# Kernel tuning notes

Measured on AMD Instinct MI355X. Metric: run time of the kernel, lower is better.

The kernel has to match this reference:

```python
import jax, jax.numpy as jnp
import numpy as np
import math

H = 4
D_MODEL = 512
OUT_DIM = D_MODEL // 2  # 256 (concat=True path)
D_K = OUT_DIM // H      # 64
N = 4096


def setup_inputs() -> dict:
    key0 = jax.random.key(0)
    ks = jax.random.split(key0, 12)
    s = 1.0 / math.sqrt(D_MODEL)
    inp = {
        "query": jax.random.normal(ks[0], (N, D_MODEL), dtype=jnp.float32),
        "key": jax.random.normal(ks[1], (N, D_MODEL), dtype=jnp.float32),
        "mask": jax.random.randint(ks[2], (N, N), 0, 2, dtype=jnp.int32),
        # 4 linears (q, k, q_v, k_v), each d_model -> out_dim
        "Wq": jax.random.normal(ks[3], (OUT_DIM, D_MODEL), dtype=jnp.float32) * s,
        "bq": jax.random.normal(ks[4], (OUT_DIM,), dtype=jnp.float32) * s,
        "Wk": jax.random.normal(ks[5], (OUT_DIM, D_MODEL), dtype=jnp.float32) * s,
        "bk": jax.random.normal(ks[6], (OUT_DIM,), dtype=jnp.float32) * s,
        "Wqv": jax.random.normal(ks[7], (OUT_DIM, D_MODEL), dtype=jnp.float32) * s,
        "bqv": jax.random.normal(ks[8], (OUT_DIM,), dtype=jnp.float32) * s,
        "Wkv": jax.random.normal(ks[9], (OUT_DIM, D_MODEL), dtype=jnp.float32) * s,
        "bkv": jax.random.normal(ks[10], (OUT_DIM,), dtype=jnp.float32) * s,
    }
    return inp


def _heads(x, W, b):
    # [N, d_model] @ W^T + b -> [N, out_dim] -> [h, N, d_k]
    y = x @ W.T + b
    return y.reshape(-1, H, D_K).transpose(1, 0, 2)


def reference(query, key, mask, Wq, bq, Wk, bk, Wqv, bqv, Wkv, bkv):
    q = _heads(query, Wq, bq)    # [h, Nq, d_k]
    k = _heads(key, Wk, bk)      # [h, Nk, d_k]
    qv = _heads(query, Wqv, bqv)  # [h, Nq, d_k]
    kv = _heads(key, Wkv, bkv)    # [h, Nk, d_k]

    scores = jnp.einsum("hqd,hkd->hqk", q, k) / math.sqrt(D_K)  # [h, Nq, Nk]
    scores = jnp.where(mask[None] == 0, jnp.float32(-1e9), scores)
    p = jax.nn.softmax(scores, axis=-1)  # attention weights per head

    # x1 = ELU(p @ k_v), x2 = ELU(p^T @ q_v); concat over heads.
    x1 = jax.nn.elu(jnp.einsum("hqk,hkd->hqd", p, kv))  # [h, Nq, d_k]
    x2 = jax.nn.elu(jnp.einsum("hqk,hqd->hkd", p, qv))  # [h, Nk, d_k]
    x1 = x1.transpose(1, 0, 2).reshape(-1, H * D_K)  # [Nq, out_dim]
    x2 = x2.transpose(1, 0, 2).reshape(-1, H * D_K)  # [Nk, out_dim]
    # Dropout omitted (inference / deterministic reference).
    return x1, x2, p
```

## Files before the change

kernel.cpp:

```cpp
#include <hip/hip_runtime.h>
#include <hip/hip_bf16.h>

#define NN 4096
#define DMODEL 512
#define ODIM 256
#define NHEAD 4
#define DKH 64
#define NKW 64

typedef __attribute__((ext_vector_type(8))) short short8;
typedef __attribute__((ext_vector_type(4))) short short4v;
typedef __attribute__((ext_vector_type(8))) __bf16 bf16x8;
typedef __attribute__((ext_vector_type(4))) float f32x4;

__device__ __forceinline__ short f2bf(float f) {
    unsigned u = __builtin_bit_cast(unsigned, f);
    u += 0x7fffu + ((u >> 16) & 1u);
    return (short)(u >> 16);
}
__device__ __forceinline__ float bf2f(short s) {
    unsigned u = ((unsigned)(unsigned short)s) << 16;
    return __builtin_bit_cast(float, u);
}
__device__ __forceinline__ f32x4 mfma16(short8 a, short8 b, f32x4 c) {
    return __builtin_amdgcn_mfma_f32_16x16x32_bf16(
        __builtin_bit_cast(bf16x8, a), __builtin_bit_cast(bf16x8, b), c, 0, 0, 0);
}

__global__ __launch_bounds__(256) void pack_mask_k(const int* __restrict__ mask,
                                                   unsigned long long* __restrict__ bits) {
    int tid = blockIdx.x * 256 + threadIdx.x;
    int wid = tid >> 6;
    int lane = tid & 63;
    int v = __builtin_nontemporal_load(mask + (size_t)wid * 64 + lane);
    unsigned long long b = __ballot(v != 0);
    if (lane == 0) bits[wid] = b;
}

__global__ __launch_bounds__(256) void proj_k(
    const float* __restrict__ Xq, const float* __restrict__ Xk,
    const float* __restrict__ Wq, const float* __restrict__ bq,
    const float* __restrict__ Wk, const float* __restrict__ bk,
    const float* __restrict__ Wqv, const float* __restrict__ bqv,
    const float* __restrict__ Wkv, const float* __restrict__ bkv,
    short* __restrict__ qh, short* __restrict__ kh,
    short* __restrict__ qvT, short* __restrict__ kvT) {
    int z = blockIdx.z;
    const float *X, *W, *B;
    short* out;
    int tr;
    float postscale = 1.f;
    switch (z) {
        case 0: X = Xq; W = Wq;  B = bq;  out = qh;  tr = 0; postscale = 0.125f; break;
        case 1: X = Xk; W = Wk;  B = bk;  out = kh;  tr = 0; break;
        case 2: X = Xq; W = Wqv; B = bqv; out = qvT; tr = 1; break;
        default: X = Xk; W = Wkv; B = bkv; out = kvT; tr = 1; break;
    }
    int lane = threadIdx.x & 63, w = threadIdx.x >> 6;
    int lr = lane & 15, lg = lane >> 4;
    int m0 = blockIdx.x * 64 + (w >> 1) * 32;
    int n0 = blockIdx.y * 64 + (w & 1) * 32;

    f32x4 acc[2][2] = {};
    for (int kk = 0; kk < DMODEL; kk += 32) {
        short8 a[2], b[2];
#pragma unroll
        for (int i = 0; i < 2; i++) {
            const float* pa = X + (size_t)(m0 + i * 16 + lr) * DMODEL + kk + lg * 8;
            const float* pb = W + (size_t)(n0 + i * 16 + lr) * DMODEL + kk + lg * 8;
            float4 a0 = *(const float4*)pa;
            float4 a1 = *(const float4*)(pa + 4);
            float4 b0 = *(const float4*)pb;
            float4 b1 = *(const float4*)(pb + 4);
            a[i][0] = f2bf(a0.x); a[i][1] = f2bf(a0.y); a[i][2] = f2bf(a0.z); a[i][3] = f2bf(a0.w);
            a[i][4] = f2bf(a1.x); a[i][5] = f2bf(a1.y); a[i][6] = f2bf(a1.z); a[i][7] = f2bf(a1.w);
            b[i][0] = f2bf(b0.x); b[i][1] = f2bf(b0.y); b[i][2] = f2bf(b0.z); b[i][3] = f2bf(b0.w);
            b[i][4] = f2bf(b1.x); b[i][5] = f2bf(b1.y); b[i][6] = f2bf(b1.z); b[i][7] = f2bf(b1.w);
        }
#pragma unroll
        for (int i = 0; i < 2; i++)
#pragma unroll
            for (int j = 0; j < 2; j++) acc[i][j] = mfma16(a[i], b[j], acc[i][j]);
    }
#pragma unroll
    for (int i = 0; i < 2; i++)
#pragma unroll
        for (int j = 0; j < 2; j++) {
            int col = n0 + j * 16 + lr;
            float bv = B[col];
            int hh = col >> 6, dk = col & 63;
#pragma unroll
            for (int r = 0; r < 4; r++) {
                int row = m0 + i * 16 + lg * 4 + r;
                short s = f2bf((acc[i][j][r] + bv) * postscale);
                if (!tr) out[((size_t)hh * NN + row) * DKH + dk] = s;
                else     out[((size_t)hh * DKH + dk) * NN + row] = s;
            }
        }
}

__global__ __launch_bounds__(512) void attn_fused_k(
    const short* __restrict__ qh, const short* __restrict__ kh, const short* __restrict__ kvT,
    const unsigned long long* __restrict__ bits,
    short* __restrict__ pbuf, float* __restrict__ linv_ws,
    float* __restrict__ x1_out, float* __restrict__ p_out) {
    int h = blockIdx.y;
    int strip = blockIdx.x;
    int tid = threadIdx.x, lane = tid & 63, w = tid >> 6;
    int lr = lane & 15, lg = lane >> 4;
    int q0 = strip * 16;

    __shared__ float smemf[4608];
    short (*plds)[16][72] = (short (*)[16][72])smemf;
    float (*xbuf)[64][17] = (float (*)[64][17])smemf;
    __shared__ float sl[8][16];
    __shared__ float linv_s[16];

    const short* khh = kh + (size_t)h * NN * DKH;
    const unsigned long long* brow = bits + (size_t)(q0 + lr) * NKW;
    short* ptile0 = pbuf + (((size_t)(h * 256 + strip) * 64) << 10);

    short8 bq[2];
#pragma unroll
    for (int kk = 0; kk < 2; kk++)
        bq[kk] = *(const short8*)(qh + ((size_t)h * NN + q0 + lr) * DKH + kk * 32 + lg * 8);

    float lrun = 0.f;
    f32x4 acc1[4] = {};
    for (int t = 0; t < 8; t++) {
        int kt = w * 8 + t;
        f32x4 s[4] = {};
#pragma unroll
        for (int fj = 0; fj < 4; fj++)
#pragma unroll
            for (int kk = 0; kk < 2; kk++) {
                short8 a = *(const short8*)(khh + (size_t)(kt * 64 + fj * 16 + lr) * DKH + kk * 32 + lg * 8);
                s[fj] = mfma16(a, bq[kk], s[fj]);
            }
        unsigned long long mw = brow[kt] >> (lg * 4);
#pragma unroll
        for (int fj = 0; fj < 4; fj++) {
            short4v pb4;
#pragma unroll
            for (int r = 0; r < 4; r++) {
                bool keep = (mw >> (fj * 16 + r)) & 1ull;
                float e = __expf(keep ? s[fj][r] : -100.f);
                lrun += e;
                pb4[r] = f2bf(e);
            }
            *(short4v*)&plds[w][lr][fj * 16 + lg * 4] = pb4;
        }
#pragma unroll
        for (int kk = 0; kk < 2; kk++) {
            short8 a1 = *(const short8*)&plds[w][lr][kk * 32 + lg * 8];
#pragma unroll
            for (int fd = 0; fd < 4; fd++) {
                short8 bv = *(const short8*)(kvT + ((size_t)h * DKH + fd * 16 + lr) * NN + kt * 64 + kk * 32 + lg * 8);
                acc1[fd] = mfma16(a1, bv, acc1[fd]);
            }
        }
        {
            short8 v0, v1;
#pragma unroll
            for (int j = 0; j < 8; j++) v0[j] = plds[w][j][lane];
#pragma unroll
            for (int j = 0; j < 8; j++) v1[j] = plds[w][8 + j][lane];
            short* ptile = ptile0 + ((size_t)kt << 10) + lane * 16;
            *(short8*)(ptile) = v0;
            *(short8*)(ptile + 8) = v1;
        }
    }
    lrun += __shfl_xor(lrun, 16);
    lrun += __shfl_xor(lrun, 32);
    if (lg == 0) sl[w][lr] = lrun;
    __syncthreads();
    float l = 0.f;
#pragma unroll
    for (int w2 = 0; w2 < 8; w2++) l += sl[w2][lr];
    float linv = l > 0.f ? 1.f / l : 0.f;
    if (w == 0 && lg == 0) {
        linv_s[lr] = linv;
        linv_ws[(size_t)h * NN + q0 + lr] = linv;
    }
    __syncthreads();

    asm volatile("s_waitcnt vmcnt(0)" ::: "memory");
    float linvv[16];
#pragma unroll
    for (int j = 0; j < 16; j++) linvv[j] = linv_s[j];
    const short* tl0 = ptile0 + ((size_t)(w * 8) << 10) + lane * 16;
    short8 pv0 = *(const short8*)(tl0);
    short8 pv1 = *(const short8*)(tl0 + 8);
    for (int t = 0; t < 8; t++) {
        int kt = w * 8 + t;
        short8 n0 = pv0, n1 = pv1;
        if (t < 7) {
            const short* tn = ptile0 + ((size_t)(kt + 1) << 10) + lane * 16;
            n0 = *(const short8*)(tn);
            n1 = *(const short8*)(tn + 8);
        }
        float* pd = p_out + ((size_t)h * NN + q0) * NN + kt * 64 + lane;
#pragma unroll
        for (int j = 0; j < 8; j++) pd[(size_t)j * NN] = bf2f(pv0[j]) * linvv[j];
#pragma unroll
        for (int j = 0; j < 8; j++) pd[(size_t)(8 + j) * NN] = bf2f(pv1[j]) * linvv[8 + j];
        pv0 = n0; pv1 = n1;
    }

    __syncthreads();
    if (w >= 4) {
#pragma unroll
        for (int fd = 0; fd < 4; fd++)
#pragma unroll
            for (int r = 0; r < 4; r++) xbuf[w - 4][lane][fd * 4 + r] = acc1[fd][r];
    }
    __syncthreads();
    if (w < 4) {
#pragma unroll
        for (int fd = 0; fd < 4; fd++)
#pragma unroll
            for (int r = 0; r < 4; r++) acc1[fd][r] += xbuf[w][lane][fd * 4 + r];
    }
    __syncthreads();
    if (w >= 1 && w < 4) {
#pragma unroll
        for (int fd = 0; fd < 4; fd++)
#pragma unroll
            for (int r = 0; r < 4; r++) xbuf[w - 1][lane][fd * 4 + r] = acc1[fd][r];
    }
    __syncthreads();
    if (w == 0) {
#pragma unroll
        for (int fd = 0; fd < 4; fd++)
#pragma unroll
            for (int r = 0; r < 4; r++) {
                float v = acc1[fd][r] + xbuf[0][lane][fd * 4 + r] + xbuf[1][lane][fd * 4 + r] +
                          xbuf[2][lane][fd * 4 + r];
                v *= linv_s[lg * 4 + r];
                v = v > 0.f ? v : (__expf(v) - 1.f);
                x1_out[(size_t)(q0 + lg * 4 + r) * ODIM + h * DKH + fd * 16 + lr] = v;
            }
    }
}

__global__ __launch_bounds__(256) void scale_qv_k(const short* __restrict__ qvT,
                                                  const float* __restrict__ linv,
                                                  short* __restrict__ qvS) {
    int idx = blockIdx.x * 256 + threadIdx.x;
    int q8 = idx & 511;
    int dh = idx >> 9;
    int h = dh >> 6;
    short8 v = *(const short8*)(qvT + (size_t)dh * NN + q8 * 8);
    const float* lp = linv + (size_t)h * NN + q8 * 8;
    float4 l0 = *(const float4*)lp;
    float4 l1 = *(const float4*)(lp + 4);
    short8 o;
    o[0] = f2bf(bf2f(v[0]) * l0.x); o[1] = f2bf(bf2f(v[1]) * l0.y);
    o[2] = f2bf(bf2f(v[2]) * l0.z); o[3] = f2bf(bf2f(v[3]) * l0.w);
    o[4] = f2bf(bf2f(v[4]) * l1.x); o[5] = f2bf(bf2f(v[5]) * l1.y);
    o[6] = f2bf(bf2f(v[6]) * l1.z); o[7] = f2bf(bf2f(v[7]) * l1.w);
    *(short8*)(qvS + (size_t)dh * NN + q8 * 8) = o;
}

__global__ __launch_bounds__(512) void px2b_k(
    const short* __restrict__ pbuf, const short* __restrict__ qvS,
    float* __restrict__ x2part) {
    int kt = blockIdx.x, h = blockIdx.y, z = blockIdx.z;
    int tid = threadIdx.x, lane = tid & 63, w = tid >> 6;
    int fj = w & 3, sh = w >> 2;
    int lr = lane & 15, lg = lane >> 4;

    __shared__ float red[4][64][17];

    const short* qvh = qvS + (size_t)h * DKH * NN;
    f32x4 acc[4] = {};
    int qbase = z * 1024 + sh * 512;

    int qq0 = qbase;
    int strip0 = (qq0 >> 4) + (lg >> 1);
    short8 afc = *(const short8*)(pbuf + (((size_t)(h * 256 + strip0) * 64 + kt) << 10) +
                                  (fj * 16 + lr) * 16 + (lg & 1) * 8);
    short8 bvc0 = *(const short8*)(qvh + (size_t)(0 * 16 + lr) * NN + qq0 + lg * 8);
    short8 bvc1 = *(const short8*)(qvh + (size_t)(1 * 16 + lr) * NN + qq0 + lg * 8);
    short8 bvc2 = *(const short8*)(qvh + (size_t)(2 * 16 + lr) * NN + qq0 + lg * 8);
    short8 bvc3 = *(const short8*)(qvh + (size_t)(3 * 16 + lr) * NN + qq0 + lg * 8);

    for (int it = 0; it < 16; it++) {
        short8 afn = afc, bvn0 = bvc0, bvn1 = bvc1, bvn2 = bvc2, bvn3 = bvc3;
        if (it < 15) {
            int qq = qbase + (it + 1) * 32;
            int strip = (qq >> 4) + (lg >> 1);
            afn = *(const short8*)(pbuf + (((size_t)(h * 256 + strip) * 64 + kt) << 10) +
                                   (fj * 16 + lr) * 16 + (lg & 1) * 8);
            bvn0 = *(const short8*)(qvh + (size_t)(0 * 16 + lr) * NN + qq + lg * 8);
            bvn1 = *(const short8*)(qvh + (size_t)(1 * 16 + lr) * NN + qq + lg * 8);
            bvn2 = *(const short8*)(qvh + (size_t)(2 * 16 + lr) * NN + qq + lg * 8);
            bvn3 = *(const short8*)(qvh + (size_t)(3 * 16 + lr) * NN + qq + lg * 8);
        }
        acc[0] = mfma16(afc, bvc0, acc[0]);
        acc[1] = mfma16(afc, bvc1, acc[1]);
        acc[2] = mfma16(afc, bvc2, acc[2]);
        acc[3] = mfma16(afc, bvc3, acc[3]);
        afc = afn; bvc0 = bvn0; bvc1 = bvn1; bvc2 = bvn2; bvc3 = bvn3;
    }
    if (sh == 1) {
#pragma unroll
        for (int fd = 0; fd < 4; fd++)
#pragma unroll
            for (int r = 0; r < 4; r++) red[fj][lane][fd * 4 + r] = acc[fd][r];
    }
    __syncthreads();
    if (sh == 0) {
        float* xp = x2part + (size_t)z * NN * ODIM;
#pragma unroll
        for (int fd = 0; fd < 4; fd++)
#pragma unroll
            for (int r = 0; r < 4; r++) {
                float v = acc[fd][r] + red[fj][lane][fd * 4 + r];
                xp[(size_t)(kt * 64 + fj * 16 + lg * 4 + r) * ODIM + h * DKH + fd * 16 + lr] = v;
            }
    }
}

__global__ __launch_bounds__(256) void combine_x2_k(const float* __restrict__ x2part,
                                                    float* __restrict__ x2_out) {
    int idx = blockIdx.x * 256 + threadIdx.x;
    size_t i = (size_t)idx * 4;
    const size_t stride = (size_t)NN * ODIM;
    float4 a = *(const float4*)(x2part + i);
    float4 b = *(const float4*)(x2part + stride + i);
    float4 c = *(const float4*)(x2part + 2 * stride + i);
    float4 d = *(const float4*)(x2part + 3 * stride + i);
    float4 o;
    o.x = a.x + b.x + c.x + d.x;
    o.y = a.y + b.y + c.y + d.y;
    o.z = a.z + b.z + c.z + d.z;
    o.w = a.w + b.w + c.w + d.w;
    o.x = o.x > 0.f ? o.x : (__expf(o.x) - 1.f);
    o.y = o.y > 0.f ? o.y : (__expf(o.y) - 1.f);
    o.z = o.z > 0.f ? o.z : (__expf(o.z) - 1.f);
    o.w = o.w > 0.f ? o.w : (__expf(o.w) - 1.f);
    *(float4*)(x2_out + i) = o;
}

__global__ __launch_bounds__(512) void attn_fb_k(
    const short* __restrict__ qh, const short* __restrict__ kh, const short* __restrict__ kvT,
    const unsigned long long* __restrict__ bits,
    float* __restrict__ x1_out, float* __restrict__ p_out) {
    int h = blockIdx.y;
    int tid = threadIdx.x, lane = tid & 63, w = tid >> 6;
    int lr = lane & 15, lg = lane >> 4;
    int q0 = blockIdx.x * 16;

    __shared__ float smemf[4608];
    short (*plds)[16][72] = (short (*)[16][72])smemf;
    float (*xbuf)[64][17] = (float (*)[64][17])smemf;
    __shared__ float sl[8][16];

    const short* khh = kh + (size_t)h * NN * DKH;
    const unsigned long long* brow = bits + (size_t)(q0 + lr) * NKW;

    short8 bq[2];
#pragma unroll
    for (int kk = 0; kk < 2; kk++)
        bq[kk] = *(const short8*)(qh + ((size_t)h * NN + q0 + lr) * DKH + kk * 32 + lg * 8);

    float lrun = 0.f;
    for (int t = 0; t < 8; t++) {
        int kt = w * 8 + t;
        f32x4 s[4] = {};
#pragma unroll
        for (int fj = 0; fj < 4; fj++)
#pragma unroll
            for (int kk = 0; kk < 2; kk++) {
                short8 a = *(const short8*)(khh + (size_t)(kt * 64 + fj * 16 + lr) * DKH + kk * 32 + lg * 8);
                s[fj] = mfma16(a, bq[kk], s[fj]);
            }
        unsigned long long mw = brow[kt] >> (lg * 4);
#pragma unroll
        for (int fj = 0; fj < 4; fj++)
#pragma unroll
            for (int r = 0; r < 4; r++) {
                bool keep = (mw >> (fj * 16 + r)) & 1ull;
                lrun += __expf(keep ? s[fj][r] : -100.f);
            }
    }
    lrun += __shfl_xor(lrun, 16);
    lrun += __shfl_xor(lrun, 32);
    if (lg == 0) sl[w][lr] = lrun;
    __syncthreads();
    float l = 0.f;
#pragma unroll
    for (int w2 = 0; w2 < 8; w2++) l += sl[w2][lr];
    float linv = l > 0.f ? 1.f / l : 0.f;

    f32x4 acc1[4] = {};
    float* prow = p_out + ((size_t)h * NN + q0 + lr) * NN;
    for (int t = 0; t < 8; t++) {
        int kt = w * 8 + t;
        f32x4 s[4] = {};
#pragma unroll
        for (int fj = 0; fj < 4; fj++)
#pragma unroll
            for (int kk = 0; kk < 2; kk++) {
                short8 a = *(const short8*)(khh + (size_t)(kt * 64 + fj * 16 + lr) * DKH + kk * 32 + lg * 8);
                s[fj] = mfma16(a, bq[kk], s[fj]);
            }
        unsigned long long mw = brow[kt] >> (lg * 4);
#pragma unroll
        for (int fj = 0; fj < 4; fj++) {
            float4 pv;
            short4v pb;
#pragma unroll
            for (int r = 0; r < 4; r++) {
                bool keep = (mw >> (fj * 16 + r)) & 1ull;
                float p = __expf(keep ? s[fj][r] : -100.f) * linv;
                (&pv.x)[r] = p;
                pb[r] = f2bf(p);
            }
            *(float4*)(prow + kt * 64 + fj * 16 + lg * 4) = pv;
            *(short4v*)&plds[w][lr][fj * 16 + lg * 4] = pb;
        }
#pragma unroll
        for (int kk = 0; kk < 2; kk++) {
            short8 a1 = *(const short8*)&plds[w][lr][kk * 32 + lg * 8];
#pragma unroll
            for (int fd = 0; fd < 4; fd++) {
                short8 bv = *(const short8*)(kvT + ((size_t)h * DKH + fd * 16 + lr) * NN + kt * 64 + kk * 32 + lg * 8);
                acc1[fd] = mfma16(a1, bv, acc1[fd]);
            }
        }
    }
    __syncthreads();
    if (w >= 4) {
#pragma unroll
        for (int fd = 0; fd < 4; fd++)
#pragma unroll
            for (int r = 0; r < 4; r++) xbuf[w - 4][lane][fd * 4 + r] = acc1[fd][r];
    }
    __syncthreads();
    if (w < 4) {
#pragma unroll
        for (int fd = 0; fd < 4; fd++)
#pragma unroll
            for (int r = 0; r < 4; r++) acc1[fd][r] += xbuf[w][lane][fd * 4 + r];
    }
    __syncthreads();
    if (w >= 1 && w < 4) {
#pragma unroll
        for (int fd = 0; fd < 4; fd++)
#pragma unroll
            for (int r = 0; r < 4; r++) xbuf[w - 1][lane][fd * 4 + r] = acc1[fd][r];
    }
    __syncthreads();
    if (w == 0) {
#pragma unroll
        for (int fd = 0; fd < 4; fd++)
#pragma unroll
            for (int r = 0; r < 4; r++) {
                float v = acc1[fd][r] + xbuf[0][lane][fd * 4 + r] + xbuf[1][lane][fd * 4 + r] +
                          xbuf[2][lane][fd * 4 + r];
                v = v > 0.f ? v : (__expf(v) - 1.f);
                x1_out[(size_t)(q0 + lg * 4 + r) * ODIM + h * DKH + fd * 16 + lr] = v;
            }
    }
}

__global__ __launch_bounds__(512) void px2_fb_k(
    const float* __restrict__ p, const short* __restrict__ qvT,
    float* __restrict__ x2_out) {
    int h = blockIdx.y;
    int k0 = blockIdx.x * 32;
    int tid = threadIdx.x, lane = tid & 63, w = tid >> 6;
    int lr = lane & 15, lg = lane >> 4;

    __shared__ float red[4][64][33];

    f32x4 acc[2][4] = {};
    const float* pbase = p + (size_t)h * NN * NN;
    const short* qvh = qvT + (size_t)h * DKH * NN;

    for (int it = 0; it < 16; it++) {
        int qq = w * 512 + it * 32;
        short8 aP[2];
#pragma unroll
        for (int fj = 0; fj < 2; fj++) {
            const float* pp = pbase + (size_t)(qq + lg * 8) * NN + k0 + fj * 16 + lr;
            short8 av;
#pragma unroll
            for (int j = 0; j < 8; j++) av[j] = f2bf(pp[j * NN]);
            aP[fj] = av;
        }
#pragma unroll
        for (int fd = 0; fd < 4; fd++) {
            short8 bv = *(const short8*)(qvh + (size_t)(fd * 16 + lr) * NN + qq + lg * 8);
#pragma unroll
            for (int fj = 0; fj < 2; fj++) acc[fj][fd] = mfma16(aP[fj], bv, acc[fj][fd]);
        }
    }
    if (w >= 4) {
#pragma unroll
        for (int fj = 0; fj < 2; fj++)
#pragma unroll
            for (int fd = 0; fd < 4; fd++)
#pragma unroll
                for (int r = 0; r < 4; r++)
                    red[w - 4][lane][fj * 16 + fd * 4 + r] = acc[fj][fd][r];
    }
    __syncthreads();
    if (w < 4) {
#pragma unroll
        for (int fj = 0; fj < 2; fj++)
#pragma unroll
            for (int fd = 0; fd < 4; fd++)
#pragma unroll
                for (int r = 0; r < 4; r++)
                    acc[fj][fd][r] += red[w][lane][fj * 16 + fd * 4 + r];
    }
    __syncthreads();
    if (w >= 1 && w < 4) {
#pragma unroll
        for (int fj = 0; fj < 2; fj++)
#pragma unroll
            for (int fd = 0; fd < 4; fd++)
#pragma unroll
                for (int r = 0; r < 4; r++)
                    red[w - 1][lane][fj * 16 + fd * 4 + r] = acc[fj][fd][r];
    }
    __syncthreads();
    if (w == 0) {
#pragma unroll
        for (int fj = 0; fj < 2; fj++)
#pragma unroll
            for (int fd = 0; fd < 4; fd++)
#pragma unroll
                for (int r = 0; r < 4; r++) {
                    float v = acc[fj][fd][r];
#pragma unroll
                    for (int s2 = 0; s2 < 3; s2++) v += red[s2][lane][fj * 16 + fd * 4 + r];
                    v = v > 0.f ? v : (__expf(v) - 1.f);
                    x2_out[(size_t)(k0 + fj * 16 + lg * 4 + r) * ODIM + h * DKH + fd * 16 + lr] = v;
                }
    }
}

extern "C" void kernel_launch(void* const* d_in, const int* in_sizes, int n_in,
                              void* d_out, int out_size, void* d_ws, size_t ws_size,
                              hipStream_t stream) {
    (void)in_sizes; (void)n_in; (void)out_size;
    const float* query = (const float*)d_in[0];
    const float* key   = (const float*)d_in[1];
    const int*   mask  = (const int*)d_in[2];
    const float* Wq  = (const float*)d_in[3];
    const float* bq  = (const float*)d_in[4];
    const float* Wk  = (const float*)d_in[5];
    const float* bk  = (const float*)d_in[6];
    const float* Wqv = (const float*)d_in[7];
    const float* bqv = (const float*)d_in[8];
    const float* Wkv = (const float*)d_in[9];
    const float* bkv = (const float*)d_in[10];

    float* out = (float*)d_out;
    float* x1 = out;
    float* x2 = out + (size_t)NN * ODIM;
    float* p  = out + (size_t)2 * NN * ODIM;

    char* ws = (char*)d_ws;
    short* qh  = (short*)(ws);
    short* kh  = (short*)(ws + (2ull << 20));
    short* qvT = (short*)(ws + (4ull << 20));
    short* kvT = (short*)(ws + (6ull << 20));
    unsigned long long* bits = (unsigned long long*)(ws + (8ull << 20));
    float* linv_ws = (float*)(ws + (10ull << 20));
    short* qvS = (short*)(ws + (10ull << 20) + (1ull << 19));
    float* x2part = (float*)(ws + (13ull << 20));
    short* pbuf = (short*)(ws + (29ull << 20));
    size_t need = (29ull << 20) + (size_t)NHEAD * NN * NN * sizeof(short);

    hipLaunchKernelGGL(pack_mask_k, dim3(NN * NN / 64 / 4), dim3(256), 0, stream, mask, bits);
    hipLaunchKernelGGL(proj_k, dim3(64, 4, 4), dim3(256), 0, stream,
                       query, key, Wq, bq, Wk, bk, Wqv, bqv, Wkv, bkv, qh, kh, qvT, kvT);

    if (ws_size >= need) {
        hipLaunchKernelGGL(attn_fused_k, dim3(NN / 16, NHEAD), dim3(512), 0, stream,
                           qh, kh, kvT, bits, pbuf, linv_ws, x1, p);
        hipLaunchKernelGGL(scale_qv_k, dim3(512), dim3(256), 0, stream, qvT, linv_ws, qvS);
        hipLaunchKernelGGL(px2b_k, dim3(NN / 64, NHEAD, 4), dim3(512), 0, stream,
                           pbuf, qvS, x2part);
        hipLaunchKernelGGL(combine_x2_k, dim3(NN * ODIM / 4 / 256), dim3(256), 0, stream,
                           x2part, x2);
    } else {
        hipLaunchKernelGGL(attn_fb_k, dim3(NN / 16, NHEAD), dim3(512), 0, stream,
                           qh, kh, kvT, bits, x1, p);
        hipLaunchKernelGGL(px2_fb_k, dim3(NN / 32, NHEAD), dim3(512), 0, stream,
                           p, qvT, x2);
    }
}
```

Baseline: 344.9 us.

## Retile px2b kernel: two key fragments per wave, four-way q split with tree reduction

The P^T·qv kernel now gives each wave two 16-row key fragments (32 keys) and splits the q range across four wave groups instead of two. Each loaded qv fragment therefore feeds twice as many MFMAs, halving the qv global loads per MFMA. The explicit software prefetch is replaced by a fully unrolled loop that leaves load scheduling to the compiler. In exchange the partial sums need a two-stage shared-memory tree reduction with extra barriers, more accumulator registers, and a larger LDS buffer.

```diff
diff --git a/kernel.cpp b/kernel.cpp
--- a/kernel.cpp
+++ b/kernel.cpp
@@ -267,58 +267,77 @@
     float* __restrict__ x2part) {
     int kt = blockIdx.x, h = blockIdx.y, z = blockIdx.z;
     int tid = threadIdx.x, lane = tid & 63, w = tid >> 6;
-    int fj = w & 3, sh = w >> 2;
+    int kg = w & 1, sh = w >> 1;
     int lr = lane & 15, lg = lane >> 4;
 
-    __shared__ float red[4][64][17];
+    __shared__ float red[4][64][33];
 
     const short* qvh = qvS + (size_t)h * DKH * NN;
-    f32x4 acc[4] = {};
-    int qbase = z * 1024 + sh * 512;
-
-    int qq0 = qbase;
-    int strip0 = (qq0 >> 4) + (lg >> 1);
-    short8 afc = *(const short8*)(pbuf + (((size_t)(h * 256 + strip0) * 64 + kt) << 10) +
-                                  (fj * 16 + lr) * 16 + (lg & 1) * 8);
-    short8 bvc0 = *(const short8*)(qvh + (size_t)(0 * 16 + lr) * NN + qq0 + lg * 8);
-    short8 bvc1 = *(const short8*)(qvh + (size_t)(1 * 16 + lr) * NN + qq0 + lg * 8);
-    short8 bvc2 = *(const short8*)(qvh + (size_t)(2 * 16 + lr) * NN + qq0 + lg * 8);
-    short8 bvc3 = *(const short8*)(qvh + (size_t)(3 * 16 + lr) * NN + qq0 + lg * 8);
-
-    for (int it = 0; it < 16; it++) {
-        short8 afn = afc, bvn0 = bvc0, bvn1 = bvc1, bvn2 = bvc2, bvn3 = bvc3;
-        if (it < 15) {
-            int qq = qbase + (it + 1) * 32;
-            int strip = (qq >> 4) + (lg >> 1);
-            afn = *(const short8*)(pbuf + (((size_t)(h * 256 + strip) * 64 + kt) << 10) +
-                                   (fj * 16 + lr) * 16 + (lg & 1) * 8);
-            bvn0 = *(const short8*)(qvh + (size_t)(0 * 16 + lr) * NN + qq + lg * 8);
-            bvn1 = *(const short8*)(qvh + (size_t)(1 * 16 + lr) * NN + qq + lg * 8);
-            bvn2 = *(const short8*)(qvh + (size_t)(2 * 16 + lr) * NN + qq + lg * 8);
-            bvn3 = *(const short8*)(qvh + (size_t)(3 * 16 + lr) * NN + qq + lg * 8);
-        }
-        acc[0] = mfma16(afc, bvc0, acc[0]);
-        acc[1] = mfma16(afc, bvc1, acc[1]);
-        acc[2] = mfma16(afc, bvc2, acc[2]);
-        acc[3] = mfma16(afc, bvc3, acc[3]);
-        afc = afn; bvc0 = bvn0; bvc1 = bvn1; bvc2 = bvn2; bvc3 = bvn3;
-    }
-    if (sh == 1) {
-#pragma unroll
-        for (int fd = 0; fd < 4; fd++)
-#pragma unroll
-            for (int r = 0; r < 4; r++) red[fj][lane][fd * 4 + r] = acc[fd][r];
-    }
-    __syncthreads();
-    if (sh == 0) {
+    f32x4 acc[2][4] = {};
+    int qz = z * 1024 + sh * 256;
+
+#pragma unroll
+    for (int it = 0; it < 8; it++) {
+        int qq = qz + it * 32;
+        int strip = (qq >> 4) + (lg >> 1);
+        const short* tb = pbuf + (((size_t)(h * 256 + strip) * 64 + kt) << 10) + (lg & 1) * 8;
+        short8 af0 = *(const short8*)(tb + (kg * 32 + lr) * 16);
+        short8 af1 = *(const short8*)(tb + (kg * 32 + 16 + lr) * 16);
+        short8 bv0 = *(const short8*)(qvh + (size_t)(0 * 16 + lr) * NN + qq + lg * 8);
+        short8 bv1 = *(const short8*)(qvh + (size_t)(1 * 16 + lr) * NN + qq + lg * 8);
+        short8 bv2 = *(const short8*)(qvh + (size_t)(2 * 16 + lr) * NN + qq + lg * 8);
+        short8 bv3 = *(const short8*)(qvh + (size_t)(3 * 16 + lr) * NN + qq + lg * 8);
+        acc[0][0] = mfma16(af0, bv0, acc[0][0]);
+        acc[0][1] = mfma16(af0, bv1, acc[0][1]);
+        acc[0][2] = mfma16(af0, bv2, acc[0][2]);
+        acc[0][3] = mfma16(af0, bv3, acc[0][3]);
+        acc[1][0] = mfma16(af1, bv0, acc[1][0]);
+        acc[1][1] = mfma16(af1, bv1, acc[1][1]);
+        acc[1][2] = mfma16(af1, bv2, acc[1][2]);
+        acc[1][3] = mfma16(af1, bv3, acc[1][3]);
+    }
+    if (w >= 4) {
+#pragma unroll
+        for (int fj2 = 0; fj2 < 2; fj2++)
+#pragma unroll
+            for (int fd = 0; fd < 4; fd++)
+#pragma unroll
+                for (int r = 0; r < 4; r++)
+                    red[w - 4][lane][fj2 * 16 + fd * 4 + r] = acc[fj2][fd][r];
+    }
+    __syncthreads();
+    if (w < 4) {
+#pragma unroll
+        for (int fj2 = 0; fj2 < 2; fj2++)
+#pragma unroll
+            for (int fd = 0; fd < 4; fd++)
+#pragma unroll
+                for (int r = 0; r < 4; r++)
+                    acc[fj2][fd][r] += red[w][lane][fj2 * 16 + fd * 4 + r];
+    }
+    __syncthreads();
+    if (w >= 2 && w < 4) {
+#pragma unroll
+        for (int fj2 = 0; fj2 < 2; fj2++)
+#pragma unroll
+            for (int fd = 0; fd < 4; fd++)
+#pragma unroll
+                for (int r = 0; r < 4; r++)
+                    red[w - 2][lane][fj2 * 16 + fd * 4 + r] = acc[fj2][fd][r];
+    }
+    __syncthreads();
+    if (w < 2) {
         float* xp = x2part + (size_t)z * NN * ODIM;
 #pragma unroll
-        for (int fd = 0; fd < 4; fd++)
-#pragma unroll
-            for (int r = 0; r < 4; r++) {
-                float v = acc[fd][r] + red[fj][lane][fd * 4 + r];
-                xp[(size_t)(kt * 64 + fj * 16 + lg * 4 + r) * ODIM + h * DKH + fd * 16 + lr] = v;
-            }
+        for (int fj2 = 0; fj2 < 2; fj2++)
+#pragma unroll
+            for (int fd = 0; fd < 4; fd++)
+#pragma unroll
+                for (int r = 0; r < 4; r++) {
+                    float v = acc[fj2][fd][r] + red[w][lane][fj2 * 16 + fd * 4 + r];
+                    int row = kt * 64 + kg * 32 + fj2 * 16 + lg * 4 + r;
+                    xp[(size_t)row * ODIM + h * DKH + fd * 16 + lr] = v;
+                }
     }
 }
 
```

Result: faster. 324.6 us (-5.9%).
